# Kernel tuning notes

Hardware: AMD Instinct MI355X
Metric: run time of the kernel (lower is better)

The kernel has to match this reference:

```python
import jax, jax.numpy as jnp
import numpy as np

D_MODEL = 1024
NUM_HEADS = 16
HEAD_DIM = D_MODEL // NUM_HEADS
B, T = 2, 2048


def setup_inputs() -> dict:
    key = jax.random.key(0)
    kx, kq, kk, kv, ko = jax.random.split(key, 5)
    s = 1.0 / np.sqrt(D_MODEL)
    x = jax.random.normal(kx, (B, T, D_MODEL), dtype=jnp.float32)
    Wq = jax.random.normal(kq, (D_MODEL, D_MODEL), dtype=jnp.float32) * s
    Wk = jax.random.normal(kk, (D_MODEL, D_MODEL), dtype=jnp.float32) * s
    Wv = jax.random.normal(kv, (D_MODEL, D_MODEL), dtype=jnp.float32) * s
    Wo = jax.random.normal(ko, (D_MODEL, D_MODEL), dtype=jnp.float32) * s
    # causal boolean mask [T,T], True = keep (every row keeps >=1 key)
    attn_mask = jnp.tril(jnp.ones((T, T), dtype=bool))
    return {"x": x, "Wq": Wq, "Wk": Wk, "Wv": Wv, "Wo": Wo, "attn_mask": attn_mask}


def reference(x, Wq, Wk, Wv, Wo, attn_mask):
    Bb, Tt, Dd = x.shape
    h, dh = NUM_HEADS, HEAD_DIM
    # Linear(bias=False): y = x @ W.T
    q = (x @ Wq.T).reshape(Bb, Tt, h, dh).transpose(0, 2, 1, 3)  # [B,h,T,dh]
    k = (x @ Wk.T).reshape(Bb, Tt, h, dh).transpose(0, 2, 1, 3)
    v = (x @ Wv.T).reshape(Bb, Tt, h, dh).transpose(0, 2, 1, 3)
    scores = jnp.einsum('bhqd,bhkd->bhqk', q, k) / jnp.sqrt(jnp.float32(dh))
    keep = attn_mask[None, None, :, :]  # [1,1,T,T], True = keep
    scores = jnp.where(keep, scores, -jnp.inf)
    # original subtracts row max then softmax; jax.nn.softmax is equivalent (stable)
    attn = jax.nn.softmax(scores, axis=-1)
    out = jnp.einsum('bhqk,bhkd->bhqd', attn, v)  # [B,h,T,dh]
    out = out.transpose(0, 2, 1, 3).reshape(Bb, Tt, Dd)
    return out @ Wo.T
```

## Files before the change

kernel.cpp:

```cpp
#include <hip/hip_runtime.h>
#include <hip/hip_bf16.h>
#include <stdint.h>

typedef __bf16 bf16_t;
typedef bf16_t bf16x4 __attribute__((ext_vector_type(4)));
typedef bf16_t bf16x8 __attribute__((ext_vector_type(8)));
typedef float  f32x4  __attribute__((ext_vector_type(4)));
typedef float  f32x16 __attribute__((ext_vector_type(16)));

#define MFMA16(a, b, c) __builtin_amdgcn_mfma_f32_16x16x32_bf16((a), (b), (c), 0, 0, 0)
#define MFMA32(a, b, c) __builtin_amdgcn_mfma_f32_32x32x16_bf16((a), (b), (c), 0, 0, 0)

static __device__ __forceinline__ unsigned short f2bf(float f) {
    __hip_bfloat16 h = __float2bfloat16(f);
    return __builtin_bit_cast(unsigned short, h);
}
static __device__ __forceinline__ unsigned int pk2(float a, float b) {
    return ((unsigned int)f2bf(b) << 16) | (unsigned int)f2bf(a);
}

static __device__ __forceinline__ void gld_lds16(const void* g, void* l) {
    __builtin_amdgcn_global_load_lds(
        (const __attribute__((address_space(1))) uint32_t*)g,
        (__attribute__((address_space(3))) uint32_t*)l, 16, 0, 0);
}

#define TT     2048
#define DM     1024
#define NH     16
#define HD     64
#define MROWS  4096

__global__ __launch_bounds__(256) void cast_f32_bf16(const float* __restrict__ src,
                                                     unsigned short* __restrict__ dst, int n4) {
    int i = blockIdx.x * 256 + threadIdx.x;
    if (i >= n4) return;
    float4 v = reinterpret_cast<const float4*>(src)[i];
    ushort4 o;
    o.x = f2bf(v.x); o.y = f2bf(v.y); o.z = f2bf(v.z); o.w = f2bf(v.w);
    reinterpret_cast<ushort4*>(dst)[i] = o;
}

template <int MODE>
__global__ __launch_bounds__(256) void gemm_bt(const unsigned short* __restrict__ A,
                                               const unsigned short* __restrict__ W,
                                               float* __restrict__ out, int N,
                                               unsigned short* __restrict__ qp,
                                               unsigned short* __restrict__ kp,
                                               unsigned short* __restrict__ vp) {
    __shared__ unsigned short lA[128 * 32];
    __shared__ unsigned short lB[128 * 32];

    const int tid = threadIdx.x;
    const int l = tid & 63;
    const int w = tid >> 6;
    const int r = l & 15;
    const int g = l >> 4;
    const int wr = w >> 1, wc = w & 1;
    const int m0 = blockIdx.x * 128, n0 = blockIdx.y * 128;

    f32x4 acc[4][4];
#pragma unroll
    for (int i = 0; i < 4; i++)
#pragma unroll
        for (int j = 0; j < 4; j++) acc[i][j] = (f32x4){0.f, 0.f, 0.f, 0.f};

    const int c0 = tid, c1 = tid + 256;
    const int row0 = c0 >> 2, col0 = (c0 & 3) * 8;
    const int row1 = c1 >> 2, col1 = (c1 & 3) * 8;
    const unsigned short* a0 = A + (m0 + row0) * 1024 + col0;
    const unsigned short* a1 = A + (m0 + row1) * 1024 + col1;
    const unsigned short* b0 = W + (n0 + row0) * 1024 + col0;
    const unsigned short* b1 = W + (n0 + row1) * 1024 + col1;
    unsigned short* la0 = lA + c0 * 8;
    unsigned short* la1 = lA + c1 * 8;
    unsigned short* lb0 = lB + c0 * 8;
    unsigned short* lb1 = lB + c1 * 8;

    for (int k0 = 0; k0 < 1024; k0 += 32) {
        gld_lds16(a0 + k0, la0);
        gld_lds16(a1 + k0, la1);
        gld_lds16(b0 + k0, lb0);
        gld_lds16(b1 + k0, lb1);
        __syncthreads();

        bf16x8 af[4], bfr[4];
#pragma unroll
        for (int i = 0; i < 4; i++)
            af[i] = *reinterpret_cast<const bf16x8*>(lA + (wr * 64 + i * 16 + r) * 32 + g * 8);
#pragma unroll
        for (int j = 0; j < 4; j++)
            bfr[j] = *reinterpret_cast<const bf16x8*>(lB + (wc * 64 + j * 16 + r) * 32 + g * 8);
#pragma unroll
        for (int i = 0; i < 4; i++)
#pragma unroll
            for (int j = 0; j < 4; j++) acc[i][j] = MFMA16(af[i], bfr[j], acc[i][j]);
        __syncthreads();
    }

#pragma unroll
    for (int i = 0; i < 4; i++) {
#pragma unroll
        for (int j = 0; j < 4; j++) {
#pragma unroll
            for (int reg = 0; reg < 4; reg++) {
                const int mg = m0 + wr * 64 + i * 16 + g * 4 + reg;
                const int ng = n0 + wc * 64 + j * 16 + r;
                const float v = acc[i][j][reg];
                if constexpr (MODE == 1) {
                    out[mg * N + ng] = v;
                } else {
                    const int sel = ng >> 10;
                    const int c10 = ng & 1023;
                    const int h = c10 >> 6, d = c10 & 63;
                    const int bb = mg >> 11, t = mg & 2047;
                    const int bh = bb * NH + h;
                    if (sel == 0)      qp[(bh * TT + t) * HD + d] = f2bf(v * 0.125f);
                    else if (sel == 1) kp[(bh * TT + t) * HD + d] = f2bf(v);
                    else               vp[(bh * HD + d) * TT + t] = f2bf(v);
                }
            }
        }
    }
}

__global__ __launch_bounds__(256) void attn_kernel(const unsigned short* __restrict__ q,
                                                   const unsigned short* __restrict__ k,
                                                   const unsigned short* __restrict__ v,
                                                   unsigned short* __restrict__ o) {
    __shared__ unsigned short lK[64 * 64];
    __shared__ unsigned short lV[64 * 64];

    const int tid = threadIdx.x;
    const int l   = tid & 63;
    const int w   = tid >> 6;
    const int c   = l & 31;
    const int hi  = l >> 5;

    const int id   = blockIdx.x;
    const int half = id >> 8;
    const int sub  = id & 255;
    const int bh   = sub >> 3;
    const int j8   = sub & 7;
    const int qt   = half ? (15 - j8) : j8;
    const int q0w  = qt * 128 + w * 32;
    const int nkt  = 2 * qt + 2;

    const unsigned short* qbase = q + (size_t)bh * TT * HD;
    const unsigned short* kbase = k + (size_t)bh * TT * HD;
    const unsigned short* vbase = v + (size_t)bh * HD * TT;

    bf16x8 qf[4];
#pragma unroll
    for (int ks = 0; ks < 4; ++ks)
        qf[ks] = *reinterpret_cast<const bf16x8*>(qbase + (q0w + c) * HD + ks * 16 + hi * 8);

    f32x16 Oacc[2];
#pragma unroll
    for (int jd = 0; jd < 2; ++jd)
#pragma unroll
        for (int e = 0; e < 16; ++e) Oacc[jd][e] = 0.f;
    float m_r = -1e30f, l_r = 0.f;

    const int cA = tid, cB = tid + 256;
    const int rA = cA >> 3, colA = (cA & 7) * 8;
    const int rB = cB >> 3, colB = (cB & 7) * 8;
    const int dstA = rA * 128 + ((colA * 2) ^ ((rA & 7) << 4));
    const int dstB = rB * 128 + ((colB & 7) == (cB & 7) ? ((colB * 2) ^ ((rB & 7) << 4)) : 0);

    uint4 ka, kb, va, vb;
    ka = *reinterpret_cast<const uint4*>(kbase + rA * HD + colA);
    kb = *reinterpret_cast<const uint4*>(kbase + rB * HD + colB);
    va = *reinterpret_cast<const uint4*>(vbase + rA * TT + colA);
    vb = *reinterpret_cast<const uint4*>(vbase + rB * TT + colB);

    const int dstB2 = rB * 128 + ((colB * 2) ^ ((rB & 7) << 4));

    for (int kt = 0; kt < nkt; ++kt) {
        const int k0 = kt * 64;
        __syncthreads();
        *reinterpret_cast<uint4*>((char*)lK + dstA)  = ka;
        *reinterpret_cast<uint4*>((char*)lK + dstB2) = kb;
        *reinterpret_cast<uint4*>((char*)lV + dstA)  = va;
        *reinterpret_cast<uint4*>((char*)lV + dstB2) = vb;
        __syncthreads();
        if (kt + 1 < nkt) {
            const int kn = k0 + 64;
            ka = *reinterpret_cast<const uint4*>(kbase + (kn + rA) * HD + colA);
            kb = *reinterpret_cast<const uint4*>(kbase + (kn + rB) * HD + colB);
            va = *reinterpret_cast<const uint4*>(vbase + rA * TT + kn + colA);
            vb = *reinterpret_cast<const uint4*>(vbase + rB * TT + kn + colB);
        }
        if (k0 > q0w + 31) continue;

        f32x16 s[2];
#pragma unroll
        for (int j = 0; j < 2; ++j) {
#pragma unroll
            for (int e = 0; e < 16; ++e) s[j][e] = 0.f;
#pragma unroll
            for (int ks = 0; ks < 4; ++ks) {
                const int row = j * 32 + c;
                bf16x8 kf = *reinterpret_cast<const bf16x8*>(
                    (char*)lK + row * 128 + (((ks * 16 + hi * 8) * 2) ^ ((row & 7) << 4)));
                s[j] = MFMA32(kf, qf[ks], s[j]);
            }
        }

        if (k0 + 63 > q0w) {
            const int qg = q0w + c;
#pragma unroll
            for (int j = 0; j < 2; ++j)
#pragma unroll
                for (int e = 0; e < 16; ++e) {
                    const int kv = k0 + j * 32 + (e & 3) + 8 * (e >> 2) + 4 * hi;
                    if (kv > qg) s[j][e] = -1e30f;
                }
        }

        float mx = s[0][0];
#pragma unroll
        for (int e = 1; e < 16; ++e) mx = fmaxf(mx, s[0][e]);
#pragma unroll
        for (int e = 0; e < 16; ++e) mx = fmaxf(mx, s[1][e]);
        mx = fmaxf(mx, __shfl_xor(mx, 32));
        const float mnew = fmaxf(m_r, mx);
        const float corr = __expf(m_r - mnew);
        float sum = 0.f;
#pragma unroll
        for (int j = 0; j < 2; ++j)
#pragma unroll
            for (int e = 0; e < 16; ++e) {
                const float p = __expf(s[j][e] - mnew);
                s[j][e] = p;
                sum += p;
            }
        sum += __shfl_xor(sum, 32);
        l_r = l_r * corr + sum;
        m_r = mnew;
#pragma unroll
        for (int jd = 0; jd < 2; ++jd)
#pragma unroll
            for (int e = 0; e < 16; ++e) Oacc[jd][e] *= corr;

        bf16x8 pa[4];
#pragma unroll
        for (int ks = 0; ks < 4; ++ks) {
            const int j = ks >> 1;
            const int base = (ks & 1) * 8;
            const unsigned int pA0 = pk2(s[j][base + 0], s[j][base + 1]);
            const unsigned int pA1 = pk2(s[j][base + 2], s[j][base + 3]);
            const unsigned int pB0 = pk2(s[j][base + 4], s[j][base + 5]);
            const unsigned int pB1 = pk2(s[j][base + 6], s[j][base + 7]);
            const unsigned int m0 = hi ? pB0 : pA0;
            const unsigned int m1 = hi ? pB1 : pA1;
            const unsigned int o0 = hi ? pA0 : pB0;
            const unsigned int o1 = hi ? pA1 : pB1;
            const unsigned int r0 = __shfl_xor(o0, 32);
            const unsigned int r1 = __shfl_xor(o1, 32);
            uint4 u;
            u.x = hi ? r0 : m0;
            u.y = hi ? r1 : m1;
            u.z = hi ? m0 : r0;
            u.w = hi ? m1 : r1;
            pa[ks] = __builtin_bit_cast(bf16x8, u);
        }

#pragma unroll
        for (int jd = 0; jd < 2; ++jd) {
#pragma unroll
            for (int ks = 0; ks < 4; ++ks) {
                const int row = jd * 32 + c;
                bf16x8 vf = *reinterpret_cast<const bf16x8*>(
                    (char*)lV + row * 128 + (((ks * 16 + hi * 8) * 2) ^ ((row & 7) << 4)));
                Oacc[jd] = MFMA32(vf, pa[ks], Oacc[jd]);
            }
        }
    }

    const int b_ = bh >> 4, h_ = bh & 15;
    const float inv = 1.f / l_r;
    const int qg = q0w + c;
    unsigned short* orow = o + ((size_t)b_ * TT + qg) * DM + h_ * HD;
#pragma unroll
    for (int jd = 0; jd < 2; ++jd)
#pragma unroll
        for (int ep = 0; ep < 8; ++ep) {
            const int e0 = ep * 2;
            const int d0 = jd * 32 + (e0 & 3) + 8 * (e0 >> 2) + 4 * hi;
            const unsigned int pkv = pk2(Oacc[jd][e0] * inv, Oacc[jd][e0 + 1] * inv);
            *reinterpret_cast<unsigned int*>(orow + d0) = pkv;
        }
}

extern "C" void kernel_launch(void* const* d_in, const int* in_sizes, int n_in,
                              void* d_out, int out_size, void* d_ws, size_t ws_size,
                              hipStream_t stream) {
    const float* x  = (const float*)d_in[0];
    const float* Wq = (const float*)d_in[1];
    const float* Wk = (const float*)d_in[2];
    const float* Wv = (const float*)d_in[3];
    const float* Wo = (const float*)d_in[4];

    char* ws = (char*)d_ws;
    unsigned short* xb   = (unsigned short*)(ws);
    unsigned short* wqkv = (unsigned short*)(ws + (8u  << 20));
    unsigned short* wo   = (unsigned short*)(ws + (14u << 20));
    unsigned short* qb   = (unsigned short*)(ws + (16u << 20));
    unsigned short* kb   = (unsigned short*)(ws + (24u << 20));
    unsigned short* vb   = (unsigned short*)(ws + (32u << 20));
    unsigned short* ab   = (unsigned short*)(ws + (40u << 20));
    float* outp = (float*)d_out;

    cast_f32_bf16<<<4096, 256, 0, stream>>>(x, xb, 1048576);
    cast_f32_bf16<<<1024, 256, 0, stream>>>(Wq, wqkv, 262144);
    cast_f32_bf16<<<1024, 256, 0, stream>>>(Wk, wqkv + (1u << 20), 262144);
    cast_f32_bf16<<<1024, 256, 0, stream>>>(Wv, wqkv + (2u << 20), 262144);
    cast_f32_bf16<<<1024, 256, 0, stream>>>(Wo, wo, 262144);

    gemm_bt<0><<<dim3(32, 24), 256, 0, stream>>>(xb, wqkv, nullptr, 3072, qb, kb, vb);
    attn_kernel<<<512, 256, 0, stream>>>(qb, kb, vb, ab);
    gemm_bt<1><<<dim3(32, 8), 256, 0, stream>>>(ab, wo, outp, 1024, nullptr, nullptr, nullptr);
}
```

Before: 233.2 us.

## Replace QKV GEMM with 8-wave 256x256 double-buffered async-LDS kernel

Adds a dedicated QKV projection kernel that gives each 512-thread block a 256x256 tile. It uses a 64-wide K step with double-buffered global_load_lds prefetch two stages ahead, an XOR-swizzled LDS layout, a tile-swizzled block order, and s_setprio around the MFMA bursts. It needs 128KB of dynamic LDS and runs one block per CU across 192 blocks. The goal is better operand reuse and hiding load latency behind MFMA work in the largest GEMM. The attention and output GEMM changes are only cleanup and renaming.

```diff
diff --git a/kernel.cpp b/kernel.cpp
--- a/kernel.cpp
+++ b/kernel.cpp
@@ -41,13 +41,118 @@
     reinterpret_cast<ushort4*>(dst)[i] = o;
 }
 
-template <int MODE>
-__global__ __launch_bounds__(256) void gemm_bt(const unsigned short* __restrict__ A,
-                                               const unsigned short* __restrict__ W,
-                                               float* __restrict__ out, int N,
-                                               unsigned short* __restrict__ qp,
-                                               unsigned short* __restrict__ kp,
-                                               unsigned short* __restrict__ vp) {
+__global__ __launch_bounds__(512, 1) void gemm_qkv_8w(const unsigned short* __restrict__ A,
+                                                      const unsigned short* __restrict__ W,
+                                                      unsigned short* __restrict__ qp,
+                                                      unsigned short* __restrict__ kp,
+                                                      unsigned short* __restrict__ vp) {
+    extern __shared__ char lds[];
+
+    const int tid = threadIdx.x;
+    const int l = tid & 63;
+    const int w = tid >> 6;
+    const int r = l & 15, g = l >> 4;
+    const int rb = r & 7;
+    const int wr = w >> 2, wc = w & 3;
+
+    const int bid = blockIdx.x;
+    const int swz = (bid & 7) * 24 + (bid >> 3);
+    const int m0 = (swz & 15) * 256;
+    const int n0 = (swz >> 4) * 256;
+
+    const int lrow = l >> 3;
+    const int gch  = (l & 7) ^ lrow;
+    const unsigned short* aG = A + (size_t)(m0 + w * 8 + lrow) * 1024 + gch * 8;
+    const unsigned short* bG = W + (size_t)(n0 + w * 8 + lrow) * 1024 + gch * 8;
+    const int lOff = (w * 64 + l) * 16;
+
+#define QKV_STAGE(t)                                                             \
+    do {                                                                         \
+        char* ab = lds + ((t) & 1) * 32768;                                      \
+        char* bb = lds + 65536 + ((t) & 1) * 32768;                              \
+        _Pragma("unroll")                                                        \
+        for (int q_ = 0; q_ < 4; ++q_) {                                         \
+            gld_lds16(aG + q_ * 65536 + (t) * 64, ab + q_ * 8192 + lOff);        \
+            gld_lds16(bG + q_ * 65536 + (t) * 64, bb + q_ * 8192 + lOff);        \
+        }                                                                        \
+    } while (0)
+
+#define SYNC_FENCE() __builtin_amdgcn_sched_barrier(0)
+
+    f32x4 acc[8][4];
+#pragma unroll
+    for (int i = 0; i < 8; i++)
+#pragma unroll
+        for (int j = 0; j < 4; j++) acc[i][j] = (f32x4){0.f, 0.f, 0.f, 0.f};
+
+    QKV_STAGE(0);
+    QKV_STAGE(1);
+    asm volatile("s_waitcnt vmcnt(8)" ::: "memory");
+    __builtin_amdgcn_s_barrier();
+    SYNC_FENCE();
+
+    const char* aRd = lds + (wr * 128 + r) * 128;
+    const char* bRd = lds + 65536 + (wc * 64 + r) * 128;
+
+    for (int t = 0; t < 16; ++t) {
+        const int boff = (t & 1) * 32768;
+#pragma unroll
+        for (int kk = 0; kk < 2; ++kk) {
+            const int ch = ((kk * 4 + g) ^ rb) * 16;
+            bf16x8 af[8], bff[4];
+#pragma unroll
+            for (int i = 0; i < 8; ++i)
+                af[i] = *reinterpret_cast<const bf16x8*>(aRd + boff + i * 2048 + ch);
+#pragma unroll
+            for (int j = 0; j < 4; ++j)
+                bff[j] = *reinterpret_cast<const bf16x8*>(bRd + boff + j * 2048 + ch);
+            __builtin_amdgcn_s_setprio(1);
+#pragma unroll
+            for (int i = 0; i < 8; ++i)
+#pragma unroll
+                for (int j = 0; j < 4; ++j) acc[i][j] = MFMA16(af[i], bff[j], acc[i][j]);
+            __builtin_amdgcn_s_setprio(0);
+        }
+        SYNC_FENCE();
+        __builtin_amdgcn_s_barrier();
+        SYNC_FENCE();
+        if (t + 2 < 16) {
+            QKV_STAGE(t + 2);
+            asm volatile("s_waitcnt vmcnt(8)" ::: "memory");
+        } else {
+            asm volatile("s_waitcnt vmcnt(0)" ::: "memory");
+        }
+        __builtin_amdgcn_s_barrier();
+        SYNC_FENCE();
+    }
+
+#pragma unroll
+    for (int i = 0; i < 8; ++i) {
+#pragma unroll
+        for (int j = 0; j < 4; ++j) {
+#pragma unroll
+            for (int reg = 0; reg < 4; ++reg) {
+                const int mg = m0 + wr * 128 + i * 16 + g * 4 + reg;
+                const int ng = n0 + wc * 64 + j * 16 + r;
+                const float v = acc[i][j][reg];
+                const int sel = ng >> 10;
+                const int c10 = ng & 1023;
+                const int h = c10 >> 6, d = c10 & 63;
+                const int bb_ = mg >> 11, tq = mg & 2047;
+                const int bh = bb_ * NH + h;
+                if (sel == 0)      qp[(bh * TT + tq) * HD + d] = f2bf(v * 0.125f);
+                else if (sel == 1) kp[(bh * TT + tq) * HD + d] = f2bf(v);
+                else               vp[(bh * HD + d) * TT + tq] = f2bf(v);
+            }
+        }
+    }
+#undef QKV_STAGE
+#undef SYNC_FENCE
+}
+
+__global__ __launch_bounds__(256) void gemm_out(const unsigned short* __restrict__ A,
+                                                const unsigned short* __restrict__ W,
+                                                float* __restrict__ out, int N) {
     __shared__ unsigned short lA[128 * 32];
     __shared__ unsigned short lB[128 * 32];
 
@@ -99,29 +204,15 @@
     }
 
 #pragma unroll
-    for (int i = 0; i < 4; i++) {
-#pragma unroll
-        for (int j = 0; j < 4; j++) {
+    for (int i = 0; i < 4; i++)
+#pragma unroll
+        for (int j = 0; j < 4; j++)
 #pragma unroll
             for (int reg = 0; reg < 4; reg++) {
                 const int mg = m0 + wr * 64 + i * 16 + g * 4 + reg;
                 const int ng = n0 + wc * 64 + j * 16 + r;
-                const float v = acc[i][j][reg];
-                if constexpr (MODE == 1) {
-                    out[mg * N + ng] = v;
-                } else {
-                    const int sel = ng >> 10;
-                    const int c10 = ng & 1023;
-                    const int h = c10 >> 6, d = c10 & 63;
-                    const int bb = mg >> 11, t = mg & 2047;
-                    const int bh = bb * NH + h;
-                    if (sel == 0)      qp[(bh * TT + t) * HD + d] = f2bf(v * 0.125f);
-                    else if (sel == 1) kp[(bh * TT + t) * HD + d] = f2bf(v);
-                    else               vp[(bh * HD + d) * TT + t] = f2bf(v);
-                }
+                out[mg * N + ng] = acc[i][j][reg];
             }
-        }
-    }
 }
 
 __global__ __launch_bounds__(256) void attn_kernel(const unsigned short* __restrict__ q,
@@ -166,7 +257,7 @@
     const int rA = cA >> 3, colA = (cA & 7) * 8;
     const int rB = cB >> 3, colB = (cB & 7) * 8;
     const int dstA = rA * 128 + ((colA * 2) ^ ((rA & 7) << 4));
-    const int dstB = rB * 128 + ((colB & 7) == (cB & 7) ? ((colB * 2) ^ ((rB & 7) << 4)) : 0);
+    const int dstB = rB * 128 + ((colB * 2) ^ ((rB & 7) << 4));
 
     uint4 ka, kb, va, vb;
     ka = *reinterpret_cast<const uint4*>(kbase + rA * HD + colA);
@@ -174,15 +265,13 @@
     va = *reinterpret_cast<const uint4*>(vbase + rA * TT + colA);
     vb = *reinterpret_cast<const uint4*>(vbase + rB * TT + colB);
 
-    const int dstB2 = rB * 128 + ((colB * 2) ^ ((rB & 7) << 4));
-
     for (int kt = 0; kt < nkt; ++kt) {
         const int k0 = kt * 64;
         __syncthreads();
-        *reinterpret_cast<uint4*>((char*)lK + dstA)  = ka;
-        *reinterpret_cast<uint4*>((char*)lK + dstB2) = kb;
-        *reinterpret_cast<uint4*>((char*)lV + dstA)  = va;
-        *reinterpret_cast<uint4*>((char*)lV + dstB2) = vb;
+        *reinterpret_cast<uint4*>((char*)lK + dstA) = ka;
+        *reinterpret_cast<uint4*>((char*)lK + dstB) = kb;
+        *reinterpret_cast<uint4*>((char*)lV + dstA) = va;
+        *reinterpret_cast<uint4*>((char*)lV + dstB) = vb;
         __syncthreads();
         if (kt + 1 < nkt) {
             const int kn = k0 + 64;
@@ -252,17 +341,17 @@
             const unsigned int pA1 = pk2(s[j][base + 2], s[j][base + 3]);
             const unsigned int pB0 = pk2(s[j][base + 4], s[j][base + 5]);
             const unsigned int pB1 = pk2(s[j][base + 6], s[j][base + 7]);
-            const unsigned int m0 = hi ? pB0 : pA0;
-            const unsigned int m1 = hi ? pB1 : pA1;
+            const unsigned int m0_ = hi ? pB0 : pA0;
+            const unsigned int m1_ = hi ? pB1 : pA1;
             const unsigned int o0 = hi ? pA0 : pB0;
             const unsigned int o1 = hi ? pA1 : pB1;
             const unsigned int r0 = __shfl_xor(o0, 32);
             const unsigned int r1 = __shfl_xor(o1, 32);
             uint4 u;
-            u.x = hi ? r0 : m0;
-            u.y = hi ? r1 : m1;
-            u.z = hi ? m0 : r0;
-            u.w = hi ? m1 : r1;
+            u.x = hi ? r0 : m0_;
+            u.y = hi ? r1 : m1_;
+            u.z = hi ? m0_ : r0;
+            u.w = hi ? m1_ : r1;
             pa[ks] = __builtin_bit_cast(bf16x8, u);
         }
 
@@ -318,7 +407,7 @@
     cast_f32_bf16<<<1024, 256, 0, stream>>>(Wv, wqkv + (2u << 20), 262144);
     cast_f32_bf16<<<1024, 256, 0, stream>>>(Wo, wo, 262144);
 
-    gemm_bt<0><<<dim3(32, 24), 256, 0, stream>>>(xb, wqkv, nullptr, 3072, qb, kb, vb);
+    gemm_qkv_8w<<<192, 512, 131072, stream>>>(xb, wqkv, qb, kb, vb);
     attn_kernel<<<512, 256, 0, stream>>>(qb, kb, vb, ab);
-    gemm_bt<1><<<dim3(32, 8), 256, 0, stream>>>(ab, wo, outp, 1024, nullptr, nullptr, nullptr);
-}
+    gemm_out<<<dim3(32, 8), 256, 0, stream>>>(ab, wo, outp, 1024);
+}
```

Measured after the change: 236.4 us. Within noise of the previous version (+1.4%).

## Rewrite projection GEMMs with double-buffered LDS, larger tiles, swizzle, fused weight casts

Applied to the files above, without the earlier changes.

Replaces the single-buffered 128x128 K=32 GEMM with a templated kernel that stages K=64 slices into double-buffered LDS via global_load_lds. It uses XOR-swizzled LDS addressing, a grid swizzle for L2 locality, and MFMA priority hints. The QKV projection now uses 256x256 tiles with 512 threads and 128 KB of dynamic LDS. The four weight-cast launches are merged into one 2D launch. The larger tiles and LDS use limit occupancy to one block per CU, and the QKV grid of 192 blocks may leave some CUs idle.

```diff
diff --git a/kernel.cpp b/kernel.cpp
--- a/kernel.cpp
+++ b/kernel.cpp
@@ -3,7 +3,6 @@
 #include <stdint.h>
 
 typedef __bf16 bf16_t;
-typedef bf16_t bf16x4 __attribute__((ext_vector_type(4)));
 typedef bf16_t bf16x8 __attribute__((ext_vector_type(8)));
 typedef float  f32x4  __attribute__((ext_vector_type(4)));
 typedef float  f32x16 __attribute__((ext_vector_type(16)));
@@ -29,10 +28,9 @@
 #define DM     1024
 #define NH     16
 #define HD     64
-#define MROWS  4096
-
-__global__ __launch_bounds__(256) void cast_f32_bf16(const float* __restrict__ src,
-                                                     unsigned short* __restrict__ dst, int n4) {
+
+__global__ __launch_bounds__(256) void cast_x(const float* __restrict__ src,
+                                              unsigned short* __restrict__ dst, int n4) {
     int i = blockIdx.x * 256 + threadIdx.x;
     if (i >= n4) return;
     float4 v = reinterpret_cast<const float4*>(src)[i];
@@ -41,83 +39,122 @@
     reinterpret_cast<ushort4*>(dst)[i] = o;
 }
 
-template <int MODE>
-__global__ __launch_bounds__(256) void gemm_bt(const unsigned short* __restrict__ A,
-                                               const unsigned short* __restrict__ W,
-                                               float* __restrict__ out, int N,
-                                               unsigned short* __restrict__ qp,
-                                               unsigned short* __restrict__ kp,
-                                               unsigned short* __restrict__ vp) {
-    __shared__ unsigned short lA[128 * 32];
-    __shared__ unsigned short lB[128 * 32];
+__global__ __launch_bounds__(256) void cast_w(const float* __restrict__ wq,
+                                              const float* __restrict__ wk,
+                                              const float* __restrict__ wv,
+                                              const float* __restrict__ wo_in,
+                                              unsigned short* __restrict__ wqkv,
+                                              unsigned short* __restrict__ wo_out) {
+    const int y = blockIdx.y;
+    const float* src = (y == 0) ? wq : (y == 1) ? wk : (y == 2) ? wv : wo_in;
+    unsigned short* dst = (y < 3) ? (wqkv + (size_t)y * (1u << 20)) : wo_out;
+    int i = blockIdx.x * 256 + threadIdx.x;
+    float4 v = reinterpret_cast<const float4*>(src)[i];
+    ushort4 o;
+    o.x = f2bf(v.x); o.y = f2bf(v.y); o.z = f2bf(v.z); o.w = f2bf(v.w);
+    reinterpret_cast<ushort4*>(dst)[i] = o;
+}
+
+template <int BM, int BN, int WM, int WN, int MODE>
+__global__ __launch_bounds__(WM * WN * 64, 1)
+void gemm2ph(const unsigned short* __restrict__ A, const unsigned short* __restrict__ W,
+             float* __restrict__ out, int Nn,
+             unsigned short* __restrict__ qp, unsigned short* __restrict__ kp,
+             unsigned short* __restrict__ vp, int gridM) {
+    constexpr int THREADS = WM * WN * 64;
+    constexpr int MF = BM / WM / 16;
+    constexpr int NF = BN / WN / 16;
+    constexpr int ABYTES = BM * 128;
+    constexpr int BUFB = ABYTES + BN * 128;
+    extern __shared__ char lds[];
 
     const int tid = threadIdx.x;
-    const int l = tid & 63;
-    const int w = tid >> 6;
-    const int r = l & 15;
-    const int g = l >> 4;
-    const int wr = w >> 1, wc = w & 1;
-    const int m0 = blockIdx.x * 128, n0 = blockIdx.y * 128;
-
-    f32x4 acc[4][4];
-#pragma unroll
-    for (int i = 0; i < 4; i++)
-#pragma unroll
-        for (int j = 0; j < 4; j++) acc[i][j] = (f32x4){0.f, 0.f, 0.f, 0.f};
-
-    const int c0 = tid, c1 = tid + 256;
-    const int row0 = c0 >> 2, col0 = (c0 & 3) * 8;
-    const int row1 = c1 >> 2, col1 = (c1 & 3) * 8;
-    const unsigned short* a0 = A + (m0 + row0) * 1024 + col0;
-    const unsigned short* a1 = A + (m0 + row1) * 1024 + col1;
-    const unsigned short* b0 = W + (n0 + row0) * 1024 + col0;
-    const unsigned short* b1 = W + (n0 + row1) * 1024 + col1;
-    unsigned short* la0 = lA + c0 * 8;
-    unsigned short* la1 = lA + c1 * 8;
-    unsigned short* lb0 = lB + c0 * 8;
-    unsigned short* lb1 = lB + c1 * 8;
-
-    for (int k0 = 0; k0 < 1024; k0 += 32) {
-        gld_lds16(a0 + k0, la0);
-        gld_lds16(a1 + k0, la1);
-        gld_lds16(b0 + k0, lb0);
-        gld_lds16(b1 + k0, lb1);
+    const int l = tid & 63, w = tid >> 6;
+    const int r = l & 15, g = l >> 4, rb = r & 7;
+    const int wm = w / WN, wn = w % WN;
+
+    const int bid = blockIdx.x;
+    const int cpx = gridDim.x >> 3;
+    const int swz = (bid & 7) * cpx + (bid >> 3);
+    const int m0 = (swz % gridM) * BM;
+    const int n0 = (swz / gridM) * BN;
+
+    const int lrow = l >> 3;
+    const int gch = (l & 7) ^ lrow;
+    const unsigned short* aG = A + (size_t)(m0 + w * 8 + lrow) * 1024 + gch * 8;
+    const unsigned short* bG = W + (size_t)(n0 + w * 8 + lrow) * 1024 + gch * 8;
+    const int lOff = (w * 64 + l) * 16;
+
+#define STAGE(buf, t)                                                              \
+    do {                                                                           \
+        char* ab_ = lds + (buf) * BUFB;                                            \
+        char* bb_ = ab_ + ABYTES;                                                  \
+        _Pragma("unroll")                                                          \
+        for (int q_ = 0; q_ < BM * 8 / THREADS; ++q_)                              \
+            gld_lds16(aG + (size_t)q_ * (THREADS / 8) * 1024 + (t) * 64,           \
+                      ab_ + q_ * THREADS * 16 + lOff);                             \
+        _Pragma("unroll")                                                          \
+        for (int q_ = 0; q_ < BN * 8 / THREADS; ++q_)                              \
+            gld_lds16(bG + (size_t)q_ * (THREADS / 8) * 1024 + (t) * 64,           \
+                      bb_ + q_ * THREADS * 16 + lOff);                             \
+    } while (0)
+
+    f32x4 acc[MF][NF];
+#pragma unroll
+    for (int i = 0; i < MF; i++)
+#pragma unroll
+        for (int j = 0; j < NF; j++) acc[i][j] = (f32x4){0.f, 0.f, 0.f, 0.f};
+
+    STAGE(0, 0);
+    __syncthreads();
+
+    int cur = 0;
+    for (int t = 0; t < 16; ++t) {
+        if (t + 1 < 16) STAGE(cur ^ 1, t + 1);
+        const char* aRd = lds + cur * BUFB + (wm * (BM / WM) + r) * 128;
+        const char* bRd = lds + cur * BUFB + ABYTES + (wn * (BN / WN) + r) * 128;
+#pragma unroll
+        for (int kk = 0; kk < 2; ++kk) {
+            const int ch = ((kk * 4 + g) ^ rb) * 16;
+            bf16x8 af[MF], bfr[NF];
+#pragma unroll
+            for (int i = 0; i < MF; ++i)
+                af[i] = *reinterpret_cast<const bf16x8*>(aRd + i * 2048 + ch);
+#pragma unroll
+            for (int j = 0; j < NF; ++j)
+                bfr[j] = *reinterpret_cast<const bf16x8*>(bRd + j * 2048 + ch);
+            __builtin_amdgcn_s_setprio(1);
+#pragma unroll
+            for (int i = 0; i < MF; ++i)
+#pragma unroll
+                for (int j = 0; j < NF; ++j) acc[i][j] = MFMA16(af[i], bfr[j], acc[i][j]);
+            __builtin_amdgcn_s_setprio(0);
+        }
         __syncthreads();
-
-        bf16x8 af[4], bfr[4];
-#pragma unroll
-        for (int i = 0; i < 4; i++)
-            af[i] = *reinterpret_cast<const bf16x8*>(lA + (wr * 64 + i * 16 + r) * 32 + g * 8);
-#pragma unroll
-        for (int j = 0; j < 4; j++)
-            bfr[j] = *reinterpret_cast<const bf16x8*>(lB + (wc * 64 + j * 16 + r) * 32 + g * 8);
-#pragma unroll
-        for (int i = 0; i < 4; i++)
-#pragma unroll
-            for (int j = 0; j < 4; j++) acc[i][j] = MFMA16(af[i], bfr[j], acc[i][j]);
-        __syncthreads();
+        cur ^= 1;
     }
-
-#pragma unroll
-    for (int i = 0; i < 4; i++) {
-#pragma unroll
-        for (int j = 0; j < 4; j++) {
-#pragma unroll
-            for (int reg = 0; reg < 4; reg++) {
-                const int mg = m0 + wr * 64 + i * 16 + g * 4 + reg;
-                const int ng = n0 + wc * 64 + j * 16 + r;
+#undef STAGE
+
+#pragma unroll
+    for (int i = 0; i < MF; ++i) {
+#pragma unroll
+        for (int j = 0; j < NF; ++j) {
+#pragma unroll
+            for (int reg = 0; reg < 4; ++reg) {
+                const int mg = m0 + wm * (BM / WM) + i * 16 + g * 4 + reg;
+                const int ng = n0 + wn * (BN / WN) + j * 16 + r;
                 const float v = acc[i][j][reg];
                 if constexpr (MODE == 1) {
-                    out[mg * N + ng] = v;
+                    out[(size_t)mg * Nn + ng] = v;
                 } else {
                     const int sel = ng >> 10;
                     const int c10 = ng & 1023;
                     const int h = c10 >> 6, d = c10 & 63;
-                    const int bb = mg >> 11, t = mg & 2047;
-                    const int bh = bb * NH + h;
-                    if (sel == 0)      qp[(bh * TT + t) * HD + d] = f2bf(v * 0.125f);
-                    else if (sel == 1) kp[(bh * TT + t) * HD + d] = f2bf(v);
-                    else               vp[(bh * HD + d) * TT + t] = f2bf(v);
+                    const int bb_ = mg >> 11, tq = mg & 2047;
+                    const int bh = bb_ * NH + h;
+                    if (sel == 0)      qp[(bh * TT + tq) * HD + d] = f2bf(v * 0.125f);
+                    else if (sel == 1) kp[(bh * TT + tq) * HD + d] = f2bf(v);
+                    else               vp[(bh * HD + d) * TT + tq] = f2bf(v);
                 }
             }
         }
@@ -166,7 +203,7 @@
     const int rA = cA >> 3, colA = (cA & 7) * 8;
     const int rB = cB >> 3, colB = (cB & 7) * 8;
     const int dstA = rA * 128 + ((colA * 2) ^ ((rA & 7) << 4));
-    const int dstB = rB * 128 + ((colB & 7) == (cB & 7) ? ((colB * 2) ^ ((rB & 7) << 4)) : 0);
+    const int dstB = rB * 128 + ((colB * 2) ^ ((rB & 7) << 4));
 
     uint4 ka, kb, va, vb;
     ka = *reinterpret_cast<const uint4*>(kbase + rA * HD + colA);
@@ -174,15 +211,13 @@
     va = *reinterpret_cast<const uint4*>(vbase + rA * TT + colA);
     vb = *reinterpret_cast<const uint4*>(vbase + rB * TT + colB);
 
-    const int dstB2 = rB * 128 + ((colB * 2) ^ ((rB & 7) << 4));
-
     for (int kt = 0; kt < nkt; ++kt) {
         const int k0 = kt * 64;
         __syncthreads();
-        *reinterpret_cast<uint4*>((char*)lK + dstA)  = ka;
-        *reinterpret_cast<uint4*>((char*)lK + dstB2) = kb;
-        *reinterpret_cast<uint4*>((char*)lV + dstA)  = va;
-        *reinterpret_cast<uint4*>((char*)lV + dstB2) = vb;
+        *reinterpret_cast<uint4*>((char*)lK + dstA) = ka;
+        *reinterpret_cast<uint4*>((char*)lK + dstB) = kb;
+        *reinterpret_cast<uint4*>((char*)lV + dstA) = va;
+        *reinterpret_cast<uint4*>((char*)lV + dstB) = vb;
         __syncthreads();
         if (kt + 1 < nkt) {
             const int kn = k0 + 64;
@@ -252,17 +287,17 @@
             const unsigned int pA1 = pk2(s[j][base + 2], s[j][base + 3]);
             const unsigned int pB0 = pk2(s[j][base + 4], s[j][base + 5]);
             const unsigned int pB1 = pk2(s[j][base + 6], s[j][base + 7]);
-            const unsigned int m0 = hi ? pB0 : pA0;
-            const unsigned int m1 = hi ? pB1 : pA1;
+            const unsigned int m0_ = hi ? pB0 : pA0;
+            const unsigned int m1_ = hi ? pB1 : pA1;
             const unsigned int o0 = hi ? pA0 : pB0;
             const unsigned int o1 = hi ? pA1 : pB1;
             const unsigned int r0 = __shfl_xor(o0, 32);
             const unsigned int r1 = __shfl_xor(o1, 32);
             uint4 u;
-            u.x = hi ? r0 : m0;
-            u.y = hi ? r1 : m1;
-            u.z = hi ? m0 : r0;
-            u.w = hi ? m1 : r1;
+            u.x = hi ? r0 : m0_;
+            u.y = hi ? r1 : m1_;
+            u.z = hi ? m0_ : r0;
+            u.w = hi ? m1_ : r1;
             pa[ks] = __builtin_bit_cast(bf16x8, u);
         }
 
@@ -312,13 +347,12 @@
     unsigned short* ab   = (unsigned short*)(ws + (40u << 20));
     float* outp = (float*)d_out;
 
-    cast_f32_bf16<<<4096, 256, 0, stream>>>(x, xb, 1048576);
-    cast_f32_bf16<<<1024, 256, 0, stream>>>(Wq, wqkv, 262144);
-    cast_f32_bf16<<<1024, 256, 0, stream>>>(Wk, wqkv + (1u << 20), 262144);
-    cast_f32_bf16<<<1024, 256, 0, stream>>>(Wv, wqkv + (2u << 20), 262144);
-    cast_f32_bf16<<<1024, 256, 0, stream>>>(Wo, wo, 262144);
-
-    gemm_bt<0><<<dim3(32, 24), 256, 0, stream>>>(xb, wqkv, nullptr, 3072, qb, kb, vb);
+    cast_x<<<4096, 256, 0, stream>>>(x, xb, 1048576);
+    cast_w<<<dim3(1024, 4), 256, 0, stream>>>(Wq, Wk, Wv, Wo, wqkv, wo);
+
+    gemm2ph<256, 256, 2, 4, 0><<<192, 512, 131072, stream>>>(
+        xb, wqkv, nullptr, 3072, qb, kb, vb, 16);
     attn_kernel<<<512, 256, 0, stream>>>(qb, kb, vb, ab);
-    gemm_bt<1><<<dim3(32, 8), 256, 0, stream>>>(ab, wo, outp, 1024, nullptr, nullptr, nullptr);
-}
+    gemm2ph<128, 128, 2, 2, 1><<<256, 256, 65536, stream>>>(
+        ab, wo, outp, 1024, nullptr, nullptr, nullptr, 32);
+}
```

Result: faster. 220.7 us (-5.3%).
